# Kernel tuning notes

Hardware: AMD Instinct MI355X
Metric: run time of the kernel (lower is better)

The kernel has to match this reference:

```python
import jax, jax.numpy as jnp
import numpy as np

EPS = 1e-8

def _dwconv1d(x, w, b):
    # x: [B, C, T], w: [C, 1, K] depthwise, b: [C]; 'same' padding
    y = jax.lax.conv_general_dilated(
        x, w, window_strides=(1,), padding='SAME',
        dimension_numbers=('NCH', 'OIH', 'NCH'),
        feature_group_count=x.shape[1])
    return y + b[None, :, None]

def _conv1d(x, w, b):
    # x: [B, 1, T], w: [1, 1, K], b: [1]
    y = jax.lax.conv_general_dilated(
        x, w, window_strides=(1,), padding='SAME',
        dimension_numbers=('NCH', 'OIH', 'NCH'))
    return y + b[None, :, None]

def setup_inputs() -> dict:
    key = jax.random.key(0)
    ks = jax.random.split(key, 8)
    B, F, T = 4, 256, 60000
    N_bands, N_diff, N_la, N_g, sigma_g = 8, 5, 11, 15, 3.0
    x = jax.random.uniform(ks[0], (B, F, T), dtype=jnp.float32)
    log_gamma = jnp.full((N_bands,), jnp.log(10.0), dtype=jnp.float32)
    # diff kernel: [-1, +1] centered, depthwise conv2d weight [8,1,1,5]
    dk = np.zeros((N_bands, 1, 1, N_diff), dtype=np.float32)
    dk[..., N_diff // 2] = -1.0
    dk[..., N_diff // 2 + 1] = 1.0
    diff_w = jnp.asarray(dk)
    diff_b = 0.01 * jax.random.normal(ks[1], (N_bands,), dtype=jnp.float32)
    la_w = jnp.ones((N_bands, 1, N_la), dtype=jnp.float32) / N_la
    la_b = 0.01 * jax.random.normal(ks[2], (N_bands,), dtype=jnp.float32)
    mix_w = jnp.ones((1, N_bands), dtype=jnp.float32) / N_bands
    gwin = jnp.exp(-(jnp.arange(N_g, dtype=jnp.float32) - N_g // 2) ** 2 / (2.0 * sigma_g))
    g_w = gwin.reshape(1, 1, -1)
    g_b = 0.01 * jax.random.normal(ks[3], (1,), dtype=jnp.float32)
    fc_w = jnp.ones((1, 4), dtype=jnp.float32) / 4.0
    fc_b = 0.01 * jax.random.normal(ks[4], (1,), dtype=jnp.float32)
    fg_w = gwin.reshape(1, 1, -1)
    fg_b = 0.01 * jax.random.normal(ks[5], (1,), dtype=jnp.float32)
    return dict(x=x, log_gamma=log_gamma, diff_w=diff_w, diff_b=diff_b,
                la_w=la_w, la_b=la_b, mix_w=mix_w, g_w=g_w, g_b=g_b,
                fc_w=fc_w, fc_b=fc_b, fg_w=fg_w, fg_b=fg_b)

def reference(x, log_gamma, diff_w, diff_b, la_w, la_b, mix_w, g_w, g_b,
              fc_w, fc_b, fg_w, fg_b):
    B, F, T = x.shape
    NB = log_gamma.shape[0]  # 8 bands
    Fb = F // NB
    # chunk(dim=1)+stack(dim=3)+permute(0,3,1,2) == reshape to [B, NB, Fb, T]
    xr = x.reshape(B, NB, Fb, T)
    # logarithmic compression, gamma per band
    xl = jnp.log1p(jnp.exp(log_gamma)[None, :, None, None] * xr)
    # depthwise temporal differentiation, kernel (1, N_diff), 'same'
    xd = jax.lax.conv_general_dilated(
        xl, diff_w, window_strides=(1, 1), padding='SAME',
        dimension_numbers=('NCHW', 'OIHW', 'NCHW'),
        feature_group_count=NB) + diff_b[None, :, None, None]
    # half-wave rectification (LeakyReLU, slope 0.0)
    xh = jax.nn.leaky_relu(xd, negative_slope=0.0)
    # pool over frequency -> [B, NB, T]
    xp = xh.sum(axis=2)
    # subtract local average (depthwise conv1d, ones/11)
    xs = xp - _dwconv1d(xp, la_w, la_b)
    # weighted sum over bands (Linear, no bias) -> [B, 1, T]
    xm = jnp.einsum('bct,oc->bot', xs, mix_w)
    # gaussian smoothing -> [B, T]
    xg = _conv1d(xm, g_w, g_b)[:, 0, :]
    xg = jax.nn.leaky_relu(xg, negative_slope=0.0)
    spectral_flux = xg / (xg.max(axis=1, keepdims=True) + EPS)
    # Fuser: concat 4 copies of spectral_flux along last axis -> [B, T, 4]
    conc = jnp.stack([spectral_flux] * 4, axis=-1)
    fm = jnp.einsum('btc,oc->bto', conc, fc_w) + fc_b  # [B, T, 1]
    fs = _conv1d(fm.transpose(0, 2, 1), fg_w, fg_b)    # [B, 1, T]
    fa = jax.nn.sigmoid(fs[:, 0, :])
    fused_nov = fa / (fa.max(axis=1, keepdims=True) + EPS)
    return spectral_flux, fused_nov
```

## Files before the change

### kernel.cpp

```cpp
#include <hip/hip_runtime.h>
#include <cmath>

#define T_LEN 60000
#define BATCH 4
#define NBANDS 8
#define FB 32
#define EPS 1e-8f

typedef float f4u __attribute__((ext_vector_type(4), aligned(4)));

__device__ __forceinline__ float logload(const float* row, int t, float gamma) {
    return (t >= 0 && t < T_LEN) ? __logf(fmaf(gamma, row[t], 1.0f)) : 0.f;
}

__global__ __launch_bounds__(256) void k1_xp(
        const float* __restrict__ x, const float* __restrict__ log_gamma,
        const float* __restrict__ diff_w, const float* __restrict__ diff_b,
        float* __restrict__ xp, int* __restrict__ mslots) {
    if (blockIdx.x == 0 && blockIdx.y == 0 && blockIdx.z == 0 && threadIdx.x < 8)
        mslots[threadIdx.x] = 0;
    const int tid = threadIdx.x;
    const int band = blockIdx.y, b = blockIdx.z;
    const int t0 = blockIdx.x * 1024 + tid * 4;
    const float gamma = __expf(log_gamma[band]);
    float dw[5];
#pragma unroll
    for (int k = 0; k < 5; ++k) dw[k] = diff_w[band * 5 + k];
    const float db = diff_b[band];
    const float* base = x + ((size_t)(b * NBANDS + band) * FB) * T_LEN;
    float acc[4] = {0.f, 0.f, 0.f, 0.f};
    const bool fast = (t0 >= 2) && (t0 + 5 < T_LEN);
    if (fast) {
#pragma unroll 4
        for (int f = 0; f < FB; ++f) {
            const float* row = base + (size_t)f * T_LEN;
            f4u va = *(const f4u*)(row + t0 - 2);
            f4u vb = *(const f4u*)(row + t0 + 2);
            float e[8];
            e[0] = __logf(fmaf(gamma, va.x, 1.f));
            e[1] = __logf(fmaf(gamma, va.y, 1.f));
            e[2] = __logf(fmaf(gamma, va.z, 1.f));
            e[3] = __logf(fmaf(gamma, va.w, 1.f));
            e[4] = __logf(fmaf(gamma, vb.x, 1.f));
            e[5] = __logf(fmaf(gamma, vb.y, 1.f));
            e[6] = __logf(fmaf(gamma, vb.z, 1.f));
            e[7] = __logf(fmaf(gamma, vb.w, 1.f));
#pragma unroll
            for (int j = 0; j < 4; ++j) {
                float xd = db;
#pragma unroll
                for (int k = 0; k < 5; ++k) xd = fmaf(dw[k], e[j + k], xd);
                acc[j] += fmaxf(xd, 0.f);
            }
        }
    } else if (t0 < T_LEN) {
        for (int f = 0; f < FB; ++f) {
            const float* row = base + (size_t)f * T_LEN;
            float e[8];
#pragma unroll
            for (int i = 0; i < 8; ++i) e[i] = logload(row, t0 - 2 + i, gamma);
#pragma unroll
            for (int j = 0; j < 4; ++j) {
                float xd = db;
#pragma unroll
                for (int k = 0; k < 5; ++k) xd = fmaf(dw[k], e[j + k], xd);
                acc[j] += fmaxf(xd, 0.f);
            }
        }
    }
    if (t0 < T_LEN) {
        float* op = xp + ((size_t)(b * NBANDS + band)) * T_LEN + t0;
        if (t0 + 3 < T_LEN) {
            *(float4*)op = make_float4(acc[0], acc[1], acc[2], acc[3]);
        } else {
#pragma unroll
            for (int j = 0; j < 4; ++j)
                if (t0 + j < T_LEN) op[j] = acc[j];
        }
    }
}

#define K2_STAGE 288
__global__ __launch_bounds__(256) void k2_xg(
        const float* __restrict__ xp,
        const float* __restrict__ la_w, const float* __restrict__ la_b,
        const float* __restrict__ mix_w, const float* __restrict__ g_w,
        const float* __restrict__ g_b,
        float* __restrict__ xg, int* __restrict__ m1_bits) {
    __shared__ float sh[NBANDS][K2_STAGE];
    __shared__ float H[NBANDS][25];
    __shared__ float red[4];
    const int tid = threadIdx.x;
    const int T0 = blockIdx.x * 256;
    const int b = blockIdx.y;
    const float* xpb = xp + (size_t)b * NBANDS * T_LEN;
    for (int idx = tid; idx < NBANDS * (K2_STAGE / 4); idx += 256) {
        int c = idx / (K2_STAGE / 4);
        int i4 = idx % (K2_STAGE / 4);
        int g = T0 - 16 + 4 * i4;
        const float* rowp = xpb + (size_t)c * T_LEN;
        float4 v;
        if (g >= 0 && g + 3 < T_LEN) {
            v = *(const float4*)(rowp + g);
        } else {
            v.x = (g + 0 >= 0 && g + 0 < T_LEN) ? rowp[g + 0] : 0.f;
            v.y = (g + 1 >= 0 && g + 1 < T_LEN) ? rowp[g + 1] : 0.f;
            v.z = (g + 2 >= 0 && g + 2 < T_LEN) ? rowp[g + 2] : 0.f;
            v.w = (g + 3 >= 0 && g + 3 < T_LEN) ? rowp[g + 3] : 0.f;
        }
        *(float4*)&sh[c][4 * i4] = v;
    }
    if (tid < 200) {
        int c = tid / 25, m = tid % 25;
        int klo = m - 14 > 0 ? m - 14 : 0;
        int khi = m < 10 ? m : 10;
        float mw = mix_w[c], s = 0.f;
        for (int k = klo; k <= khi; ++k)
            s += g_w[m - k] * (mw * ((k == 5 ? 1.f : 0.f) - la_w[c * 11 + k]));
        H[c][m] = s;
    }
    float Sg = 0.f;
#pragma unroll
    for (int j = 0; j < 15; ++j) Sg += g_w[j];
    float C0 = 0.f;
#pragma unroll
    for (int c = 0; c < NBANDS; ++c) C0 -= mix_w[c] * la_b[c];
    const float cst = g_b[0] + Sg * C0;
    __syncthreads();
    const int t = T0 + tid;
    float v = cst;
#pragma unroll 1
    for (int c = 0; c < NBANDS; ++c) {
        float a = 0.f;
#pragma unroll
        for (int m = 0; m < 25; ++m) a = fmaf(H[c][m], sh[c][tid + 4 + m], a);
        v += a;
    }
    if (t < 7 || (t >= T_LEN - 7 && t < T_LEN)) {
        v = g_b[0];
        for (int jj = 0; jj < 15; ++jj) {
            int tp = t + jj - 7;
            if (tp < 0 || tp >= T_LEN) continue;
            float xm = C0;
            for (int c = 0; c < NBANDS; ++c) {
                float mw = mix_w[c];
                for (int k = 0; k < 11; ++k) {
                    int i = tp + k + 11 - T0;
                    xm = fmaf(mw * ((k == 5 ? 1.f : 0.f) - la_w[c * 11 + k]),
                              sh[c][i], xm);
                }
            }
            v = fmaf(g_w[jj], xm, v);
        }
    }
    float vmax = 0.f;
    if (t < T_LEN) {
        v = fmaxf(v, 0.f);
        xg[(size_t)b * T_LEN + t] = v;
        vmax = v;
    }
#pragma unroll
    for (int off = 32; off > 0; off >>= 1) vmax = fmaxf(vmax, __shfl_down(vmax, off));
    if ((tid & 63) == 0) red[tid >> 6] = vmax;
    __syncthreads();
    if (tid == 0) {
        float m = fmaxf(fmaxf(red[0], red[1]), fmaxf(red[2], red[3]));
        atomicMax(&m1_bits[b], __float_as_int(m));
    }
}

__global__ __launch_bounds__(256) void k3a(
        const float* __restrict__ xg, const int* __restrict__ m1_bits,
        const float* __restrict__ fc_w, const float* __restrict__ fc_b,
        const float* __restrict__ fg_w, const float* __restrict__ fg_b,
        float* __restrict__ sf_out, float* __restrict__ fa_out,
        int* __restrict__ m2_bits) {
    __shared__ float shfm[272];
    __shared__ float red[4];
    const int tid = threadIdx.x;
    const int t0 = blockIdx.x * 256;
    const int b = blockIdx.y;
    const float inv = 1.f / (__int_as_float(m1_bits[b]) + EPS);
    const float sfc = fc_w[0] + fc_w[1] + fc_w[2] + fc_w[3];
    const float fcb = fc_b[0];
    for (int i = tid; i < 270; i += 256) {
        int tt = t0 + i - 7;
        float v = 0.f;
        if (tt >= 0 && tt < T_LEN)
            v = fmaf(sfc, xg[(size_t)b * T_LEN + tt] * inv, fcb);
        shfm[i] = v;
    }
    __syncthreads();
    const int t = t0 + tid;
    float fs = fg_b[0];
#pragma unroll
    for (int k = 0; k < 15; ++k) fs = fmaf(fg_w[k], shfm[tid + k], fs);
    float sig = 1.f / (1.f + __expf(-fs));
    float v;
    if (t < T_LEN) {
        sf_out[(size_t)b * T_LEN + t] = xg[(size_t)b * T_LEN + t] * inv;
        fa_out[(size_t)b * T_LEN + t] = sig;
        v = sig;
    } else {
        v = 0.f;
    }
#pragma unroll
    for (int off = 32; off > 0; off >>= 1) v = fmaxf(v, __shfl_down(v, off));
    if ((tid & 63) == 0) red[tid >> 6] = v;
    __syncthreads();
    if (tid == 0) {
        float m = fmaxf(fmaxf(red[0], red[1]), fmaxf(red[2], red[3]));
        atomicMax(&m2_bits[b], __float_as_int(m));
    }
}

__global__ void k3b(float* __restrict__ fa, const int* __restrict__ m2_bits) {
    int idx = blockIdx.x * 256 + threadIdx.x;
    if (idx >= BATCH * T_LEN) return;
    int b = idx / T_LEN;
    float inv = 1.f / (__int_as_float(m2_bits[b]) + EPS);
    fa[idx] = fa[idx] * inv;
}

extern "C" void kernel_launch(void* const* d_in, const int* in_sizes, int n_in,
                              void* d_out, int out_size, void* d_ws, size_t ws_size,
                              hipStream_t stream) {
    const float* x    = (const float*)d_in[0];
    const float* lg   = (const float*)d_in[1];
    const float* dw   = (const float*)d_in[2];
    const float* db   = (const float*)d_in[3];
    const float* law  = (const float*)d_in[4];
    const float* lab  = (const float*)d_in[5];
    const float* mixw = (const float*)d_in[6];
    const float* gw   = (const float*)d_in[7];
    const float* gb   = (const float*)d_in[8];
    const float* fcw  = (const float*)d_in[9];
    const float* fcb  = (const float*)d_in[10];
    const float* fgw  = (const float*)d_in[11];
    const float* fgb  = (const float*)d_in[12];

    float* ws = (float*)d_ws;
    float* xp = ws;
    float* xg = ws + (size_t)BATCH * NBANDS * T_LEN;
    int*   m1 = (int*)(xg + (size_t)BATCH * T_LEN);

    float* sf_out = (float*)d_out;
    float* fn_out = sf_out + (size_t)BATCH * T_LEN;

    const int tb256 = (T_LEN + 255) / 256;

    k1_xp<<<dim3((T_LEN + 1023) / 1024, NBANDS, BATCH), dim3(256), 0, stream>>>(
        x, lg, dw, db, xp, m1);
    k2_xg<<<dim3(tb256, BATCH), dim3(256), 0, stream>>>(
        xp, law, lab, mixw, gw, gb, xg, m1);
    k3a<<<dim3(tb256, BATCH), dim3(256), 0, stream>>>(
        xg, m1, fcw, fcb, fgw, fgb, sf_out, fn_out, m1 + 4);
    k3b<<<dim3((BATCH * T_LEN + 255) / 256), dim3(256), 0, stream>>>(fn_out, m1 + 4);
}
```

Baseline: 436.6 us.

## Remove redundant halo logs in k1 via wave shuffles and split frequency rows across waves

```diff
diff --git a/kernel.cpp b/kernel.cpp
--- a/kernel.cpp
+++ b/kernel.cpp
@@ -6,8 +6,6 @@
 #define NBANDS 8
 #define FB 32
 #define EPS 1e-8f
-
-typedef float f4u __attribute__((ext_vector_type(4), aligned(4)));
 
 __device__ __forceinline__ float logload(const float* row, int t, float gamma) {
     return (t >= 0 && t < T_LEN) ? __logf(fmaf(gamma, row[t], 1.0f)) : 0.f;
@@ -19,63 +17,90 @@
         float* __restrict__ xp, int* __restrict__ mslots) {
     if (blockIdx.x == 0 && blockIdx.y == 0 && blockIdx.z == 0 && threadIdx.x < 8)
         mslots[threadIdx.x] = 0;
-    const int tid = threadIdx.x;
+    __shared__ float sh[4][512];
+    const int tid = threadIdx.x, lane = tid & 63, w = tid >> 6;
     const int band = blockIdx.y, b = blockIdx.z;
-    const int t0 = blockIdx.x * 1024 + tid * 4;
+    const int tile0 = blockIdx.x * 512;
+    const int t0 = tile0 + lane * 8;
     const float gamma = __expf(log_gamma[band]);
     float dw[5];
 #pragma unroll
     for (int k = 0; k < 5; ++k) dw[k] = diff_w[band * 5 + k];
     const float db = diff_b[band];
-    const float* base = x + ((size_t)(b * NBANDS + band) * FB) * T_LEN;
-    float acc[4] = {0.f, 0.f, 0.f, 0.f};
-    const bool fast = (t0 >= 2) && (t0 + 5 < T_LEN);
-    if (fast) {
-#pragma unroll 4
-        for (int f = 0; f < FB; ++f) {
-            const float* row = base + (size_t)f * T_LEN;
-            f4u va = *(const f4u*)(row + t0 - 2);
-            f4u vb = *(const f4u*)(row + t0 + 2);
-            float e[8];
-            e[0] = __logf(fmaf(gamma, va.x, 1.f));
-            e[1] = __logf(fmaf(gamma, va.y, 1.f));
-            e[2] = __logf(fmaf(gamma, va.z, 1.f));
-            e[3] = __logf(fmaf(gamma, va.w, 1.f));
-            e[4] = __logf(fmaf(gamma, vb.x, 1.f));
-            e[5] = __logf(fmaf(gamma, vb.y, 1.f));
-            e[6] = __logf(fmaf(gamma, vb.z, 1.f));
-            e[7] = __logf(fmaf(gamma, vb.w, 1.f));
-#pragma unroll
-            for (int j = 0; j < 4; ++j) {
+    const float* row = x + ((size_t)((b * NBANDS + band) * FB + w * 8)) * T_LEN;
+    float acc[8] = {0.f, 0.f, 0.f, 0.f, 0.f, 0.f, 0.f, 0.f};
+
+    if (tile0 + 512 <= T_LEN) {
+        float4 c0 = *(const float4*)(row + t0);
+        float4 c1 = *(const float4*)(row + t0 + 4);
+#pragma unroll
+        for (int ff = 0; ff < 8; ++ff) {
+            const float* nrow = row + T_LEN;
+            float4 n0 = c0, n1 = c1;
+            if (ff < 7) {
+                n0 = *(const float4*)(nrow + t0);
+                n1 = *(const float4*)(nrow + t0 + 4);
+            }
+            float lv[8];
+            lv[0] = __logf(fmaf(gamma, c0.x, 1.f));
+            lv[1] = __logf(fmaf(gamma, c0.y, 1.f));
+            lv[2] = __logf(fmaf(gamma, c0.z, 1.f));
+            lv[3] = __logf(fmaf(gamma, c0.w, 1.f));
+            lv[4] = __logf(fmaf(gamma, c1.x, 1.f));
+            lv[5] = __logf(fmaf(gamma, c1.y, 1.f));
+            lv[6] = __logf(fmaf(gamma, c1.z, 1.f));
+            lv[7] = __logf(fmaf(gamma, c1.w, 1.f));
+            float l2 = __shfl_up(lv[6], 1);
+            float l1 = __shfl_up(lv[7], 1);
+            float r0 = __shfl_down(lv[0], 1);
+            float r1 = __shfl_down(lv[1], 1);
+            if (lane == 0)       { l2 = logload(row, t0 - 2, gamma); l1 = logload(row, t0 - 1, gamma); }
+            else if (lane == 63) { r0 = logload(row, t0 + 8, gamma); r1 = logload(row, t0 + 9, gamma); }
+            float e[12] = {l2, l1, lv[0], lv[1], lv[2], lv[3], lv[4], lv[5], lv[6], lv[7], r0, r1};
+#pragma unroll
+            for (int j = 0; j < 8; ++j) {
                 float xd = db;
 #pragma unroll
                 for (int k = 0; k < 5; ++k) xd = fmaf(dw[k], e[j + k], xd);
                 acc[j] += fmaxf(xd, 0.f);
             }
-        }
-    } else if (t0 < T_LEN) {
-        for (int f = 0; f < FB; ++f) {
-            const float* row = base + (size_t)f * T_LEN;
-            float e[8];
-#pragma unroll
-            for (int i = 0; i < 8; ++i) e[i] = logload(row, t0 - 2 + i, gamma);
-#pragma unroll
-            for (int j = 0; j < 4; ++j) {
+            row = nrow; c0 = n0; c1 = n1;
+        }
+    } else {
+        for (int ff = 0; ff < 8; ++ff) {
+            float e[12];
+#pragma unroll
+            for (int i = 0; i < 12; ++i) e[i] = logload(row, t0 - 2 + i, gamma);
+#pragma unroll
+            for (int j = 0; j < 8; ++j) {
                 float xd = db;
 #pragma unroll
                 for (int k = 0; k < 5; ++k) xd = fmaf(dw[k], e[j + k], xd);
                 acc[j] += fmaxf(xd, 0.f);
             }
-        }
-    }
-    if (t0 < T_LEN) {
-        float* op = xp + ((size_t)(b * NBANDS + band)) * T_LEN + t0;
-        if (t0 + 3 < T_LEN) {
-            *(float4*)op = make_float4(acc[0], acc[1], acc[2], acc[3]);
-        } else {
-#pragma unroll
-            for (int j = 0; j < 4; ++j)
-                if (t0 + j < T_LEN) op[j] = acc[j];
+            row += T_LEN;
+        }
+    }
+    *(float4*)&sh[w][lane * 8]     = make_float4(acc[0], acc[1], acc[2], acc[3]);
+    *(float4*)&sh[w][lane * 8 + 4] = make_float4(acc[4], acc[5], acc[6], acc[7]);
+    __syncthreads();
+    if (tid < 128) {
+        const int i = tid * 4;
+        const int t = tile0 + i;
+        float4 s0 = *(const float4*)&sh[0][i];
+        float4 s1 = *(const float4*)&sh[1][i];
+        float4 s2 = *(const float4*)&sh[2][i];
+        float4 s3 = *(const float4*)&sh[3][i];
+        float4 o = make_float4(s0.x + s1.x + s2.x + s3.x,
+                               s0.y + s1.y + s2.y + s3.y,
+                               s0.z + s1.z + s2.z + s3.z,
+                               s0.w + s1.w + s2.w + s3.w);
+        float* op = xp + ((size_t)(b * NBANDS + band)) * T_LEN + t;
+        if (t + 4 <= T_LEN) {
+            *(float4*)op = o;
+        } else if (t < T_LEN) {
+            const float* of = (const float*)&o;
+            for (int j = 0; j < 4 && t + j < T_LEN; ++j) op[j] = of[j];
         }
     }
 }
@@ -249,7 +274,7 @@
 
     const int tb256 = (T_LEN + 255) / 256;
 
-    k1_xp<<<dim3((T_LEN + 1023) / 1024, NBANDS, BATCH), dim3(256), 0, stream>>>(
+    k1_xp<<<dim3((T_LEN + 511) / 512, NBANDS, BATCH), dim3(256), 0, stream>>>(
         x, lg, dw, db, xp, m1);
     k2_xg<<<dim3(tb256, BATCH), dim3(256), 0, stream>>>(
         xp, law, lab, mixw, gw, gb, xg, m1);
```

New measurement: 429.1 us. Within noise of the previous version (-1.7%).

## Stage x tiles through shared memory in the log-diff band pooling kernel

Applied to the files above, without the earlier changes.

```diff
diff --git a/kernel.cpp b/kernel.cpp
--- a/kernel.cpp
+++ b/kernel.cpp
@@ -7,76 +7,79 @@
 #define FB 32
 #define EPS 1e-8f
 
-typedef float f4u __attribute__((ext_vector_type(4), aligned(4)));
-
-__device__ __forceinline__ float logload(const float* row, int t, float gamma) {
-    return (t >= 0 && t < T_LEN) ? __logf(fmaf(gamma, row[t], 1.0f)) : 0.f;
-}
+#define K1_TILE 496
+#define K1_ROWLEN 512
+#define K1_NBX ((T_LEN + K1_TILE - 1) / K1_TILE)
 
 __global__ __launch_bounds__(256) void k1_xp(
         const float* __restrict__ x, const float* __restrict__ log_gamma,
         const float* __restrict__ diff_w, const float* __restrict__ diff_b,
         float* __restrict__ xp, int* __restrict__ mslots) {
-    if (blockIdx.x == 0 && blockIdx.y == 0 && blockIdx.z == 0 && threadIdx.x < 8)
-        mslots[threadIdx.x] = 0;
+    extern __shared__ float sh[];
     const int tid = threadIdx.x;
-    const int band = blockIdx.y, b = blockIdx.z;
-    const int t0 = blockIdx.x * 1024 + tid * 4;
+    const int bx = blockIdx.x, band = blockIdx.y, b = blockIdx.z;
+    if (bx == 0 && band == 0 && b == 0 && tid < 8)
+        mslots[tid] = 0;
+    const int tile0 = bx * K1_TILE;
+    const int w0 = tile0 - 8;
+    const float* base = x + ((size_t)((b * NBANDS + band) * FB)) * T_LEN;
+    const bool interior = (w0 >= 0) && (w0 + K1_ROWLEN <= T_LEN);
+    if (interior) {
+#pragma unroll
+        for (int c = 0; c < 16; ++c) {
+            const int idx = c * 1024 + tid * 4;
+            const int r = idx >> 9;
+            const int i = idx & 511;
+            float4 v = *(const float4*)(base + (size_t)r * T_LEN + w0 + i);
+            *(float4*)&sh[idx] = v;
+        }
+    } else {
+        for (int c = 0; c < 16; ++c) {
+            const int idx = c * 1024 + tid * 4;
+            const int r = idx >> 9;
+            const int i = idx & 511;
+            const float* rowp = base + (size_t)r * T_LEN;
+#pragma unroll
+            for (int j = 0; j < 4; ++j) {
+                const int t = w0 + i + j;
+                sh[idx + j] = (t >= 0 && t < T_LEN) ? rowp[t] : 0.f;
+            }
+        }
+    }
+    __syncthreads();
     const float gamma = __expf(log_gamma[band]);
     float dw[5];
 #pragma unroll
     for (int k = 0; k < 5; ++k) dw[k] = diff_w[band * 5 + k];
     const float db = diff_b[band];
-    const float* base = x + ((size_t)(b * NBANDS + band) * FB) * T_LEN;
-    float acc[4] = {0.f, 0.f, 0.f, 0.f};
-    const bool fast = (t0 >= 2) && (t0 + 5 < T_LEN);
-    if (fast) {
+    const int t0 = tile0 + 2 * tid;
+    if (tid < 248 && t0 < T_LEN) {
+        float acc0 = 0.f, acc1 = 0.f;
+        const int i0 = 2 * tid + 6;
 #pragma unroll 4
-        for (int f = 0; f < FB; ++f) {
-            const float* row = base + (size_t)f * T_LEN;
-            f4u va = *(const f4u*)(row + t0 - 2);
-            f4u vb = *(const f4u*)(row + t0 + 2);
-            float e[8];
-            e[0] = __logf(fmaf(gamma, va.x, 1.f));
-            e[1] = __logf(fmaf(gamma, va.y, 1.f));
-            e[2] = __logf(fmaf(gamma, va.z, 1.f));
-            e[3] = __logf(fmaf(gamma, va.w, 1.f));
-            e[4] = __logf(fmaf(gamma, vb.x, 1.f));
-            e[5] = __logf(fmaf(gamma, vb.y, 1.f));
-            e[6] = __logf(fmaf(gamma, vb.z, 1.f));
-            e[7] = __logf(fmaf(gamma, vb.w, 1.f));
-#pragma unroll
-            for (int j = 0; j < 4; ++j) {
-                float xd = db;
-#pragma unroll
-                for (int k = 0; k < 5; ++k) xd = fmaf(dw[k], e[j + k], xd);
-                acc[j] += fmaxf(xd, 0.f);
-            }
-        }
-    } else if (t0 < T_LEN) {
-        for (int f = 0; f < FB; ++f) {
-            const float* row = base + (size_t)f * T_LEN;
-            float e[8];
-#pragma unroll
-            for (int i = 0; i < 8; ++i) e[i] = logload(row, t0 - 2 + i, gamma);
-#pragma unroll
-            for (int j = 0; j < 4; ++j) {
-                float xd = db;
-#pragma unroll
-                for (int k = 0; k < 5; ++k) xd = fmaf(dw[k], e[j + k], xd);
-                acc[j] += fmaxf(xd, 0.f);
-            }
-        }
-    }
-    if (t0 < T_LEN) {
+        for (int r = 0; r < FB; ++r) {
+            const float* rp = &sh[r * K1_ROWLEN];
+            float2 pa = *(const float2*)(rp + i0);
+            float2 pb = *(const float2*)(rp + i0 + 2);
+            float2 pc = *(const float2*)(rp + i0 + 4);
+            float e0 = __logf(fmaf(gamma, pa.x, 1.f));
+            float e1 = __logf(fmaf(gamma, pa.y, 1.f));
+            float e2 = __logf(fmaf(gamma, pb.x, 1.f));
+            float e3 = __logf(fmaf(gamma, pb.y, 1.f));
+            float e4 = __logf(fmaf(gamma, pc.x, 1.f));
+            float e5 = __logf(fmaf(gamma, pc.y, 1.f));
+            float xd0 = db, xd1 = db;
+            xd0 = fmaf(dw[0], e0, xd0); xd1 = fmaf(dw[0], e1, xd1);
+            xd0 = fmaf(dw[1], e1, xd0); xd1 = fmaf(dw[1], e2, xd1);
+            xd0 = fmaf(dw[2], e2, xd0); xd1 = fmaf(dw[2], e3, xd1);
+            xd0 = fmaf(dw[3], e3, xd0); xd1 = fmaf(dw[3], e4, xd1);
+            xd0 = fmaf(dw[4], e4, xd0); xd1 = fmaf(dw[4], e5, xd1);
+            acc0 += fmaxf(xd0, 0.f);
+            acc1 += fmaxf(xd1, 0.f);
+        }
         float* op = xp + ((size_t)(b * NBANDS + band)) * T_LEN + t0;
-        if (t0 + 3 < T_LEN) {
-            *(float4*)op = make_float4(acc[0], acc[1], acc[2], acc[3]);
-        } else {
-#pragma unroll
-            for (int j = 0; j < 4; ++j)
-                if (t0 + j < T_LEN) op[j] = acc[j];
-        }
+        op[0] = acc0;
+        if (t0 + 1 < T_LEN) op[1] = acc1;
     }
 }
 
@@ -249,7 +252,8 @@
 
     const int tb256 = (T_LEN + 255) / 256;
 
-    k1_xp<<<dim3((T_LEN + 1023) / 1024, NBANDS, BATCH), dim3(256), 0, stream>>>(
+    k1_xp<<<dim3(K1_NBX, NBANDS, BATCH), dim3(256),
+            FB * K1_ROWLEN * sizeof(float), stream>>>(
         x, lg, dw, db, xp, m1);
     k2_xg<<<dim3(tb256, BATCH), dim3(256), 0, stream>>>(
         xp, law, lab, mixw, gw, gb, xg, m1);
```

After: 412.8 us. -5.5%, faster.
